# Performance work log

Measured on AMD Instinct MI355X. Metric: run time of the kernel, lower is better.

Reference implementation:

```python
import jax, jax.numpy as jnp
import numpy as np

D = 32          # d_model
OUT = 2         # output_dim ('binding', 'radius')
PMAX = 118      # static max proton count (replaces data-dependent amax)
NMAX = 236     # static max neutron count
B = 1 << 20


def setup_inputs() -> dict:
    key = jax.random.key(0)
    ks = jax.random.split(key, 16)
    protons = jax.random.randint(ks[0], (B,), 1, PMAX + 1, dtype=jnp.int32)
    neutrons = jax.random.randint(ks[1], (B,), 1, NMAX + 1, dtype=jnp.int32)
    x = jnp.stack([protons, neutrons], axis=1)  # [B, 2]
    s = 1.0 / np.sqrt(D)
    inp = {
        "x": x,
        "embeddings": jax.random.normal(ks[2], (2, D), jnp.float32) * s,
        "Wp": jax.random.normal(ks[3], (D, D), jnp.float32) * s,
        "bp": jax.random.normal(ks[4], (D,), jnp.float32) * s,
        "Wn": jax.random.normal(ks[5], (D, D), jnp.float32) * s,
        "bn": jax.random.normal(ks[6], (D,), jnp.float32) * s,
        "W1": jax.random.normal(ks[7], (D, 2 * D), jnp.float32) * (1.0 / np.sqrt(2 * D)),
        "b1": jax.random.normal(ks[8], (D,), jnp.float32) * s,
        "ln_g": jnp.ones((D,), jnp.float32),
        "ln_b": jnp.zeros((D,), jnp.float32),
        "W2": jax.random.normal(ks[9], (D, D), jnp.float32) * s,
        "b2": jax.random.normal(ks[10], (D,), jnp.float32) * s,
        "Wr": jax.random.normal(ks[11], (OUT, D), jnp.float32) * s,
        "br": jax.random.normal(ks[12], (OUT,), jnp.float32) * s,
    }
    return inp


def _silu(v):
    return v * jax.nn.sigmoid(v)


def _chain(W, b, p0, length):
    # sequential recurrence p_t = Linear(SiLU(p_{t-1})); stack all states
    def step(p, _):
        p = _silu(p) @ W.T + b
        return p, p
    _, states = jax.lax.scan(step, p0, None, length=length)
    return states  # [length, D]


def _layernorm(h, g, b, eps=1e-5):
    mu = jnp.mean(h, axis=-1, keepdims=True)
    var = jnp.mean(jnp.square(h - mu), axis=-1, keepdims=True)
    return (h - mu) * jax.lax.rsqrt(var + eps) * g + b


def reference(x, embeddings, Wp, bp, Wn, bn, W1, b1, ln_g, ln_b, W2, b2, Wr, br):
    p_states = _chain(Wp, bp, embeddings[0], PMAX)   # [PMAX, D]
    n_states = _chain(Wn, bn, embeddings[1], NMAX)   # [NMAX, D]
    pf = p_states[x[:, 0] - 1]                       # [B, D]
    nf = n_states[x[:, 1] - 1]                       # [B, D]
    h = jnp.concatenate([pf, nf], axis=1)            # [B, 2D]
    h = h @ W1.T + b1                                # Linear(2D -> D)
    h = _silu(h)
    h = _layernorm(h, ln_g, ln_b)
    h = h @ W2.T + b2                                # Linear(D -> D)
    return h @ Wr.T + br                             # readout [B, OUT]
```

## Files before the change

### kernel.cpp

```cpp
#include <hip/hip_runtime.h>
#include <hip/hip_bf16.h>

#define DD 32
#define P_MAX 118
#define N_MAX 236
#define TBL (P_MAX * N_MAX)

typedef int   ivec4 __attribute__((ext_vector_type(4)));
typedef float fvec4 __attribute__((ext_vector_type(4)));

#define PST 0
#define NST (P_MAX * DD)
#define UOF ((P_MAX + N_MAX) * DD)
#define VOF (UOF + DD * P_MAX)
#define TOF (VOF + DD * N_MAX)

__global__ __launch_bounds__(64) void chain_kernel(
    const float* __restrict__ emb,
    const float* __restrict__ Wp, const float* __restrict__ bp,
    const float* __restrict__ Wn, const float* __restrict__ bn,
    float* __restrict__ ws)
{
    const int lane = threadIdx.x;
    const int ch = lane & 31;

    const float* W;
    const float* b;
    const float* e0;
    float* out;
    int len;
    if (blockIdx.x == 0) {
        W = Wp; b = bp; e0 = emb;       out = ws + PST; len = P_MAX;
    } else {
        W = Wn; b = bn; e0 = emb + DD;  out = ws + NST; len = N_MAX;
    }

    float w[32];
#pragma unroll
    for (int q = 0; q < 8; ++q) {
        float4 v = reinterpret_cast<const float4*>(W + ch * 32)[q];
        w[4 * q + 0] = v.x; w[4 * q + 1] = v.y;
        w[4 * q + 2] = v.z; w[4 * q + 3] = v.w;
    }
    const float bias = b[ch];
    float p = e0[ch];

    for (int t = 0; t < len; ++t) {
        float e = __expf(-p);
        float s = p * __builtin_amdgcn_rcpf(1.0f + e);
        int sb = __float_as_int(s);

        float a0 = 0.0f, a1 = 0.0f, a2 = 0.0f, a3 = 0.0f;
#pragma unroll
        for (int k = 0; k < 32; k += 4) {
            a0 += __int_as_float(__builtin_amdgcn_readlane(sb, k + 0)) * w[k + 0];
            a1 += __int_as_float(__builtin_amdgcn_readlane(sb, k + 1)) * w[k + 1];
            a2 += __int_as_float(__builtin_amdgcn_readlane(sb, k + 2)) * w[k + 2];
            a3 += __int_as_float(__builtin_amdgcn_readlane(sb, k + 3)) * w[k + 3];
        }
        p = bias + ((a0 + a1) + (a2 + a3));
        if (lane < 32) out[t * DD + ch] = p;
    }
}

__global__ __launch_bounds__(64) void uv_kernel(
    const float* __restrict__ ws_in,
    const float* __restrict__ W1, const float* __restrict__ b1,
    float* __restrict__ ws_out)
{
    const int j = blockIdx.y;
    const int bx = blockIdx.x;
    const int lane = threadIdx.x;
    const bool prot = bx < 2;
    const int t = prot ? bx * 64 + lane : (bx - 2) * 64 + lane;
    const int len = prot ? P_MAX : N_MAX;
    if (t >= len) return;

    const float* st = ws_in + (prot ? PST : NST) + t * DD;
    const float* wr = W1 + j * 64 + (prot ? 0 : 32);
    float acc = prot ? 0.0f : b1[j];
#pragma unroll
    for (int q = 0; q < 8; ++q) {
        float4 s4 = reinterpret_cast<const float4*>(st)[q];
        acc = fmaf(s4.x, wr[4 * q + 0], acc);
        acc = fmaf(s4.y, wr[4 * q + 1], acc);
        acc = fmaf(s4.z, wr[4 * q + 2], acc);
        acc = fmaf(s4.w, wr[4 * q + 3], acc);
    }
    if (prot) ws_out[UOF + j * P_MAX + t] = acc;
    else      ws_out[VOF + j * N_MAX + t] = acc;
}

__global__ __launch_bounds__(64, 1) void table_kernel(
    const float* __restrict__ ws,
    const float* __restrict__ ln_g, const float* __restrict__ ln_b,
    const float* __restrict__ W2, const float* __restrict__ b2,
    const float* __restrict__ Wr, const float* __restrict__ br,
    float2* __restrict__ table)
{
    const int e = blockIdx.x * 64 + threadIdx.x;
    if (e >= TBL) return;
    const int pi = e / N_MAX;
    const int ni = e - pi * N_MAX;

    const float* UT = ws + UOF;
    const float* VT = ws + VOF;

    float h[32];
    float mu = 0.0f;
#pragma unroll
    for (int j = 0; j < 32; ++j) {
        float a = UT[j * P_MAX + pi] + VT[j * N_MAX + ni];
        float ee = __expf(-a);
        float s = a * __builtin_amdgcn_rcpf(1.0f + ee);
        h[j] = s;
        mu += s;
    }
    mu *= (1.0f / 32.0f);
    float var = 0.0f;
#pragma unroll
    for (int j = 0; j < 32; ++j) {
        float d = h[j] - mu;
        var = fmaf(d, d, var);
    }
    var *= (1.0f / 32.0f);
    const float inv = __builtin_amdgcn_rsqf(var + 1e-5f);
#pragma unroll
    for (int j = 0; j < 32; ++j)
        h[j] = (h[j] - mu) * inv * ln_g[j] + ln_b[j];

    float h2[32];
#pragma unroll
    for (int j0 = 0; j0 < 32; j0 += 8) {
        float acc[8];
#pragma unroll
        for (int u = 0; u < 8; ++u) acc[u] = b2[j0 + u];
#pragma unroll
        for (int k = 0; k < 32; ++k) {
#pragma unroll
            for (int u = 0; u < 8; ++u)
                acc[u] = fmaf(h[k], W2[(j0 + u) * 32 + k], acc[u]);
        }
#pragma unroll
        for (int u = 0; u < 8; ++u) h2[j0 + u] = acc[u];
    }

    float o0 = br[0], o1 = br[1];
    float p0 = 0.0f, p1 = 0.0f;
#pragma unroll
    for (int k = 0; k < 32; k += 2) {
        o0 = fmaf(h2[k], Wr[k], o0);
        p0 = fmaf(h2[k + 1], Wr[k + 1], p0);
        o1 = fmaf(h2[k], Wr[32 + k], o1);
        p1 = fmaf(h2[k + 1], Wr[32 + k + 1], p1);
    }
    table[e] = make_float2(o0 + p0, o1 + p1);
}

__global__ __launch_bounds__(256) void gather_kernel(
    const ivec4* __restrict__ x4,
    const float2* __restrict__ table,
    fvec4* __restrict__ out4,
    int B4)
{
    const int i = blockIdx.x * 256 + threadIdx.x;
    if (i >= B4) return;
    ivec4 a = __builtin_nontemporal_load(x4 + 2 * i);
    ivec4 b = __builtin_nontemporal_load(x4 + 2 * i + 1);
    float2 t0 = table[(a.x - 1) * N_MAX + (a.y - 1)];
    float2 t1 = table[(a.z - 1) * N_MAX + (a.w - 1)];
    float2 t2 = table[(b.x - 1) * N_MAX + (b.y - 1)];
    float2 t3 = table[(b.z - 1) * N_MAX + (b.w - 1)];
    fvec4 o0v = {t0.x, t0.y, t1.x, t1.y};
    fvec4 o1v = {t2.x, t2.y, t3.x, t3.y};
    __builtin_nontemporal_store(o0v, out4 + 2 * i);
    __builtin_nontemporal_store(o1v, out4 + 2 * i + 1);
}

extern "C" void kernel_launch(void* const* d_in, const int* in_sizes, int n_in,
                              void* d_out, int out_size, void* d_ws, size_t ws_size,
                              hipStream_t stream) {
    const int*   x    = (const int*)d_in[0];
    const float* emb  = (const float*)d_in[1];
    const float* Wp   = (const float*)d_in[2];
    const float* bp   = (const float*)d_in[3];
    const float* Wn   = (const float*)d_in[4];
    const float* bn   = (const float*)d_in[5];
    const float* W1   = (const float*)d_in[6];
    const float* b1   = (const float*)d_in[7];
    const float* ln_g = (const float*)d_in[8];
    const float* ln_b = (const float*)d_in[9];
    const float* W2   = (const float*)d_in[10];
    const float* b2   = (const float*)d_in[11];
    const float* Wr   = (const float*)d_in[12];
    const float* br   = (const float*)d_in[13];

    const int B = in_sizes[0] / 2;

    float* wsf = (float*)d_ws;
    float2* table = (float2*)(wsf + TOF);

    chain_kernel<<<2, 64, 0, stream>>>(emb, Wp, bp, Wn, bn, wsf);

    uv_kernel<<<dim3(6, 32), 64, 0, stream>>>(wsf, W1, b1, wsf);

    table_kernel<<<(TBL + 63) / 64, 64, 0, stream>>>(
        wsf, ln_g, ln_b, W2, b2, Wr, br, table);

    gather_kernel<<<(B / 4 + 255) / 256, 256, 0, stream>>>(
        (const ivec4*)x, table, (fvec4*)d_out, B / 4);
}
```

Measured before the change: 138.3 us.

## Fold LayerNorm affine, W2 and readout into a precomputed 2x32 matrix; fuse chain+uv

Because everything after the LayerNorm is linear, ln_g, ln_b, W2, b2, Wr and br are folded into a 2x32 matrix plus per-output sums and constants. That matrix is computed once, so each table entry needs only two 32-long dot products instead of a 32x32 matvec. The recurrence chain and the W1 projection are merged into one kernel that keeps the states in shared memory, removing a launch and a global round trip. The trade-off is a slightly different floating-point summation order, and the serial chain now runs inside a 256-thread block.

```diff
diff --git a/kernel.cpp b/kernel.cpp
--- a/kernel.cpp
+++ b/kernel.cpp
@@ -9,93 +9,126 @@
 typedef int   ivec4 __attribute__((ext_vector_type(4)));
 typedef float fvec4 __attribute__((ext_vector_type(4)));
 
-#define PST 0
-#define NST (P_MAX * DD)
-#define UOF ((P_MAX + N_MAX) * DD)
-#define VOF (UOF + DD * P_MAX)
-#define TOF (VOF + DD * N_MAX)
-
-__global__ __launch_bounds__(64) void chain_kernel(
+#define UOF 0
+#define VOF (DD * P_MAX)
+#define MOF (VOF + DD * N_MAX)
+#define TOF (MOF + 68)
+
+__global__ __launch_bounds__(256) void chain_uv_kernel(
     const float* __restrict__ emb,
     const float* __restrict__ Wp, const float* __restrict__ bp,
     const float* __restrict__ Wn, const float* __restrict__ bn,
-    float* __restrict__ ws)
-{
-    const int lane = threadIdx.x;
-    const int ch = lane & 31;
-
-    const float* W;
-    const float* b;
-    const float* e0;
-    float* out;
-    int len;
-    if (blockIdx.x == 0) {
-        W = Wp; b = bp; e0 = emb;       out = ws + PST; len = P_MAX;
-    } else {
-        W = Wn; b = bn; e0 = emb + DD;  out = ws + NST; len = N_MAX;
-    }
-
-    float w[32];
-#pragma unroll
-    for (int q = 0; q < 8; ++q) {
-        float4 v = reinterpret_cast<const float4*>(W + ch * 32)[q];
-        w[4 * q + 0] = v.x; w[4 * q + 1] = v.y;
-        w[4 * q + 2] = v.z; w[4 * q + 3] = v.w;
-    }
-    const float bias = b[ch];
-    float p = e0[ch];
-
-    for (int t = 0; t < len; ++t) {
-        float e = __expf(-p);
-        float s = p * __builtin_amdgcn_rcpf(1.0f + e);
-        int sb = __float_as_int(s);
-
-        float a0 = 0.0f, a1 = 0.0f, a2 = 0.0f, a3 = 0.0f;
-#pragma unroll
-        for (int k = 0; k < 32; k += 4) {
-            a0 += __int_as_float(__builtin_amdgcn_readlane(sb, k + 0)) * w[k + 0];
-            a1 += __int_as_float(__builtin_amdgcn_readlane(sb, k + 1)) * w[k + 1];
-            a2 += __int_as_float(__builtin_amdgcn_readlane(sb, k + 2)) * w[k + 2];
-            a3 += __int_as_float(__builtin_amdgcn_readlane(sb, k + 3)) * w[k + 3];
-        }
-        p = bias + ((a0 + a1) + (a2 + a3));
-        if (lane < 32) out[t * DD + ch] = p;
-    }
-}
-
-__global__ __launch_bounds__(64) void uv_kernel(
-    const float* __restrict__ ws_in,
     const float* __restrict__ W1, const float* __restrict__ b1,
-    float* __restrict__ ws_out)
-{
-    const int j = blockIdx.y;
-    const int bx = blockIdx.x;
-    const int lane = threadIdx.x;
-    const bool prot = bx < 2;
-    const int t = prot ? bx * 64 + lane : (bx - 2) * 64 + lane;
-    const int len = prot ? P_MAX : N_MAX;
-    if (t >= len) return;
-
-    const float* st = ws_in + (prot ? PST : NST) + t * DD;
-    const float* wr = W1 + j * 64 + (prot ? 0 : 32);
-    float acc = prot ? 0.0f : b1[j];
-#pragma unroll
-    for (int q = 0; q < 8; ++q) {
-        float4 s4 = reinterpret_cast<const float4*>(st)[q];
-        acc = fmaf(s4.x, wr[4 * q + 0], acc);
-        acc = fmaf(s4.y, wr[4 * q + 1], acc);
-        acc = fmaf(s4.z, wr[4 * q + 2], acc);
-        acc = fmaf(s4.w, wr[4 * q + 3], acc);
-    }
-    if (prot) ws_out[UOF + j * P_MAX + t] = acc;
-    else      ws_out[VOF + j * N_MAX + t] = acc;
-}
-
-__global__ __launch_bounds__(64, 1) void table_kernel(
-    const float* __restrict__ ws,
     const float* __restrict__ ln_g, const float* __restrict__ ln_b,
     const float* __restrict__ W2, const float* __restrict__ b2,
     const float* __restrict__ Wr, const float* __restrict__ br,
+    float* __restrict__ ws)
+{
+    __shared__ __align__(16) float st[N_MAX * DD];
+    __shared__ float m2s[64];
+    __shared__ float mraw[64];
+
+    const int tid = threadIdx.x;
+    const bool prot = (blockIdx.x == 0);
+    const int len = prot ? P_MAX : N_MAX;
+
+    if (tid < 64) {
+        const int ch = tid & 31;
+        const float* W = prot ? Wp : Wn;
+        const float* bb = prot ? bp : bn;
+
+        float w[32];
+#pragma unroll
+        for (int q = 0; q < 8; ++q) {
+            float4 v = reinterpret_cast<const float4*>(W + ch * 32)[q];
+            w[4 * q + 0] = v.x; w[4 * q + 1] = v.y;
+            w[4 * q + 2] = v.z; w[4 * q + 3] = v.w;
+        }
+        const float bias = bb[ch];
+        float p = (prot ? emb : emb + DD)[ch];
+
+        for (int t = 0; t < len; ++t) {
+            float e = __expf(-p);
+            float s = p * __builtin_amdgcn_rcpf(1.0f + e);
+            int sb = __float_as_int(s);
+
+            float a0 = bias, a1 = 0.0f, a2 = 0.0f, a3 = 0.0f;
+#pragma unroll
+            for (int k = 0; k < 32; k += 4) {
+                a0 += __int_as_float(__builtin_amdgcn_readlane(sb, k + 0)) * w[k + 0];
+                a1 += __int_as_float(__builtin_amdgcn_readlane(sb, k + 1)) * w[k + 1];
+                a2 += __int_as_float(__builtin_amdgcn_readlane(sb, k + 2)) * w[k + 2];
+                a3 += __int_as_float(__builtin_amdgcn_readlane(sb, k + 3)) * w[k + 3];
+            }
+            p = (a0 + a1) + (a2 + a3);
+            st[t * DD + ch] = p;
+        }
+    }
+    __syncthreads();
+
+    {
+        const int j = tid & 31;
+        const int t0 = tid >> 5;
+        const float* w1row = W1 + j * 64 + (prot ? 0 : 32);
+        float wr[32];
+#pragma unroll
+        for (int q = 0; q < 8; ++q) {
+            float4 v = reinterpret_cast<const float4*>(w1row)[q];
+            wr[4 * q + 0] = v.x; wr[4 * q + 1] = v.y;
+            wr[4 * q + 2] = v.z; wr[4 * q + 3] = v.w;
+        }
+        const float base = prot ? 0.0f : b1[j];
+        float* op = ws + (prot ? UOF : VOF) + j * len;
+
+        for (int t = t0; t < len; t += 8) {
+            const float* sp = st + t * DD;
+            float acc = base;
+#pragma unroll
+            for (int q = 0; q < 8; ++q) {
+                float4 s4 = *reinterpret_cast<const float4*>(sp + 4 * q);
+                acc = fmaf(s4.x, wr[4 * q + 0], acc);
+                acc = fmaf(s4.y, wr[4 * q + 1], acc);
+                acc = fmaf(s4.z, wr[4 * q + 2], acc);
+                acc = fmaf(s4.w, wr[4 * q + 3], acc);
+            }
+            op[t] = acc;
+        }
+    }
+
+    if (prot) {
+        if (tid < 64) {
+            const int r = tid >> 5;
+            const int k = tid & 31;
+            float acc = 0.0f;
+#pragma unroll
+            for (int jj = 0; jj < 32; ++jj)
+                acc = fmaf(Wr[r * 32 + jj], W2[jj * 32 + k], acc);
+            mraw[tid] = acc;
+            const float m2 = acc * ln_g[k];
+            m2s[tid] = m2;
+            ws[MOF + tid] = m2;
+        }
+        __syncthreads();
+        if (tid < 2) {
+            const int r = tid;
+            float S = 0.0f, cb = 0.0f;
+#pragma unroll
+            for (int k = 0; k < 32; ++k) {
+                S += m2s[r * 32 + k];
+                cb = fmaf(mraw[r * 32 + k], ln_b[k], cb);
+            }
+            float c = br[r] + cb;
+#pragma unroll
+            for (int jj = 0; jj < 32; ++jj)
+                c = fmaf(Wr[r * 32 + jj], b2[jj], c);
+            ws[MOF + 64 + r] = S;
+            ws[MOF + 66 + r] = c;
+        }
+    }
+}
+
+__global__ __launch_bounds__(64, 1) void table_kernel(
+    const float* __restrict__ ws,
     float2* __restrict__ table)
 {
     const int e = blockIdx.x * 64 + threadIdx.x;
@@ -105,6 +138,7 @@
 
     const float* UT = ws + UOF;
     const float* VT = ws + VOF;
+    const float* M2 = ws + MOF;
 
     float h[32];
     float mu = 0.0f;
@@ -125,36 +159,17 @@
     }
     var *= (1.0f / 32.0f);
     const float inv = __builtin_amdgcn_rsqf(var + 1e-5f);
-#pragma unroll
-    for (int j = 0; j < 32; ++j)
-        h[j] = (h[j] - mu) * inv * ln_g[j] + ln_b[j];
-
-    float h2[32];
-#pragma unroll
-    for (int j0 = 0; j0 < 32; j0 += 8) {
-        float acc[8];
-#pragma unroll
-        for (int u = 0; u < 8; ++u) acc[u] = b2[j0 + u];
-#pragma unroll
-        for (int k = 0; k < 32; ++k) {
-#pragma unroll
-            for (int u = 0; u < 8; ++u)
-                acc[u] = fmaf(h[k], W2[(j0 + u) * 32 + k], acc[u]);
-        }
-#pragma unroll
-        for (int u = 0; u < 8; ++u) h2[j0 + u] = acc[u];
-    }
-
-    float o0 = br[0], o1 = br[1];
-    float p0 = 0.0f, p1 = 0.0f;
-#pragma unroll
-    for (int k = 0; k < 32; k += 2) {
-        o0 = fmaf(h2[k], Wr[k], o0);
-        p0 = fmaf(h2[k + 1], Wr[k + 1], p0);
-        o1 = fmaf(h2[k], Wr[32 + k], o1);
-        p1 = fmaf(h2[k + 1], Wr[32 + k + 1], p1);
-    }
-    table[e] = make_float2(o0 + p0, o1 + p1);
+
+    float d0 = 0.0f, d1 = 0.0f;
+#pragma unroll
+    for (int k = 0; k < 32; ++k) {
+        d0 = fmaf(M2[k],      h[k], d0);
+        d1 = fmaf(M2[32 + k], h[k], d1);
+    }
+    const float S0 = M2[64], S1 = M2[65];
+    const float c0 = M2[66], c1 = M2[67];
+    table[e] = make_float2(inv * (d0 - mu * S0) + c0,
+                           inv * (d1 - mu * S1) + c1);
 }
 
 __global__ __launch_bounds__(256) void gather_kernel(
@@ -200,12 +215,10 @@
     float* wsf = (float*)d_ws;
     float2* table = (float2*)(wsf + TOF);
 
-    chain_kernel<<<2, 64, 0, stream>>>(emb, Wp, bp, Wn, bn, wsf);
-
-    uv_kernel<<<dim3(6, 32), 64, 0, stream>>>(wsf, W1, b1, wsf);
-
-    table_kernel<<<(TBL + 63) / 64, 64, 0, stream>>>(
-        wsf, ln_g, ln_b, W2, b2, Wr, br, table);
+    chain_uv_kernel<<<2, 256, 0, stream>>>(
+        emb, Wp, bp, Wn, bn, W1, b1, ln_g, ln_b, W2, b2, Wr, br, wsf);
+
+    table_kernel<<<(TBL + 63) / 64, 64, 0, stream>>>(wsf, table);
 
     gather_kernel<<<(B / 4 + 255) / 256, 256, 0, stream>>>(
         (const ivec4*)x, table, (fvec4*)d_out, B / 4);
```

Measured after the change: 124.7 us. 9.9% less time.
